# Kernel optimization log

Measured on AMD Instinct MI355X. Metric: run time of the kernel, lower is better.

## Reference

```python
import jax, jax.numpy as jnp
import numpy as np

NUM_CLASSES = 1000
DIM = 256
N = 400000
MOMENTUM = 0.9


def setup_inputs() -> dict:
    key = jax.random.key(0)
    k1, k2, k3 = jax.random.split(key, 3)
    grads = jax.random.normal(k1, (N, DIM), dtype=jnp.float32)
    labels = jax.random.randint(k2, (N,), 0, NUM_CLASSES)
    # centroids buffer in its steady (initialized=True) state
    centroids = jax.random.normal(k3, (NUM_CLASSES, DIM), dtype=jnp.float32) * 0.1
    return {"grads": grads, "labels": labels, "centroids": centroids}


def reference(grads, labels, centroids):
    # --- update_centroids: per-class masked mean + EMA, as one segment-reduce ---
    sums = jax.ops.segment_sum(grads, labels, num_segments=NUM_CLASSES)            # [C, D]
    counts = jax.ops.segment_sum(jnp.ones((grads.shape[0],), grads.dtype), labels,
                                 num_segments=NUM_CLASSES)                          # [C]
    class_means = sums / jnp.maximum(counts, 1.0)[:, None]                          # [C, D]
    present = (counts > 0)[:, None]
    new_centroids = jnp.where(present,
                              MOMENTUM * centroids + (1.0 - MOMENTUM) * class_means,
                              centroids)                                            # classes with no samples keep old centroid

    # --- purify: rank-1 projection removing the first principal direction ---
    centered = new_centroids - new_centroids.mean(axis=0, keepdims=True)            # [C, D]
    _, _, Vh = jnp.linalg.svd(centered, full_matrices=False)
    v_y = Vh[0]                                                                     # [D]
    proj = (grads @ v_y)[:, None] * v_y[None, :]                                    # [N, D]
    return grads - proj
```

## Files before the change

### kernel.cpp

```cpp
#include <hip/hip_runtime.h>

#define N_ROWS 400000
#define DIM 256
#define NCLS 1000
#define NSQ 6
#define NPOLISH 8

#define NB_S 256
#define NT_S 512
#define NBE  64
#define NTE  1024
#define NB_P 2048
#define NT_P 256
#define TOTW_P (NB_P * (NT_P / 64))

typedef float f4 __attribute__((ext_vector_type(4)));

#define OFF_BAR     0
#define OFF_BAR2    64
#define OFF_COUNTS  1024
#define OFF_COLSUM  5120
#define OFF_MAXBUF  6144
#define ZERO_BYTES  6208
#define OFF_BASE    6208
#define OFF_CURSOR  10304
#define OFF_V       14400
#define OFF_IDX     15424
#define OFF_NC      1615424
#define OFF_NCT     2639424
#define OFF_MA      3663424
#define OFF_MB      3925568

template <int NBLK>
__device__ __forceinline__ void grid_bar(unsigned* bar, int& phase) {
  __syncthreads();
  if (threadIdx.x == 0) {
    ++phase;
    __threadfence();
    __hip_atomic_fetch_add(bar, 1u, __ATOMIC_RELAXED, __HIP_MEMORY_SCOPE_AGENT);
    const unsigned target = (unsigned)NBLK * (unsigned)phase;
    while (__hip_atomic_load(bar, __ATOMIC_RELAXED, __HIP_MEMORY_SCOPE_AGENT) < target)
      __builtin_amdgcn_s_sleep(8);
    __threadfence();
  }
  __syncthreads();
}

__global__ __launch_bounds__(NT_S) void k_sort(const int* __restrict__ labels,
                                               char* __restrict__ ws) {
  unsigned* bar    = (unsigned*)(ws + OFF_BAR);
  unsigned* counts = (unsigned*)(ws + OFF_COUNTS);
  unsigned* base   = (unsigned*)(ws + OFF_BASE);
  unsigned* cursor = (unsigned*)(ws + OFF_CURSOR);
  unsigned* idx    = (unsigned*)(ws + OFF_IDX);

  __shared__ unsigned su[1024];
  const int t = threadIdx.x, b = blockIdx.x;
  int phase = 0;

  for (int i = t; i < NCLS; i += NT_S) su[i] = 0u;
  __syncthreads();
  for (int i = b*NT_S + t; i < N_ROWS; i += NB_S*NT_S)
    atomicAdd(&su[labels[i]], 1u);
  __syncthreads();
  for (int i = t; i < NCLS; i += NT_S) { unsigned v = su[i]; if (v) atomicAdd(&counts[i], v); }
  grid_bar<NB_S>(bar, phase);

  if (b == 0) {
    su[t] = counts[t]; su[t+512] = counts[t+512];
    int offset = 1;
    for (int d = 512; d > 0; d >>= 1) {
      __syncthreads();
      if (t < d) { int ai = offset*(2*t+1)-1, bi = offset*(2*t+2)-1; su[bi] += su[ai]; }
      offset <<= 1;
    }
    __syncthreads();
    if (t == 0) su[1023] = 0u;
    for (int d = 1; d < 1024; d <<= 1) {
      offset >>= 1;
      __syncthreads();
      if (t < d) { int ai = offset*(2*t+1)-1, bi = offset*(2*t+2)-1;
                   unsigned tm = su[ai]; su[ai] = su[bi]; su[bi] += tm; }
    }
    __syncthreads();
    base[t] = su[t]; cursor[t] = su[t];
    base[t+512] = su[t+512]; cursor[t+512] = su[t+512];
  }
  grid_bar<NB_S>(bar, phase);

  for (int i = b*NT_S + t; i < N_ROWS; i += NB_S*NT_S) {
    unsigned p = atomicAdd(&cursor[labels[i]], 1u);
    idx[p] = (unsigned)i;
  }
}

__global__ __launch_bounds__(512) void k_reduce(const float* __restrict__ grads,
                                                const unsigned* __restrict__ idx,
                                                const unsigned* __restrict__ base,
                                                const unsigned* __restrict__ counts,
                                                const float* __restrict__ centroids,
                                                float* __restrict__ NC,
                                                float* __restrict__ NCT,
                                                float* __restrict__ colsum) {
  const int cls = blockIdx.x;
  const unsigned s0 = base[cls], n = counts[cls];
  const int wave = threadIdx.x >> 6, lane = threadIdx.x & 63;
  const f4* g4 = (const f4*)grads;
  f4 acc = {0.f, 0.f, 0.f, 0.f};
  unsigned u = (unsigned)wave;
  for (; u + 56 < n; u += 64) {
    unsigned r0 = idx[s0+u],    r1 = idx[s0+u+8];
    unsigned r2 = idx[s0+u+16], r3 = idx[s0+u+24];
    unsigned r4 = idx[s0+u+32], r5 = idx[s0+u+40];
    unsigned r6 = idx[s0+u+48], r7 = idx[s0+u+56];
    f4 a0 = g4[(size_t)r0*64 + lane];
    f4 a1 = g4[(size_t)r1*64 + lane];
    f4 a2 = g4[(size_t)r2*64 + lane];
    f4 a3 = g4[(size_t)r3*64 + lane];
    f4 a4 = g4[(size_t)r4*64 + lane];
    f4 a5 = g4[(size_t)r5*64 + lane];
    f4 a6 = g4[(size_t)r6*64 + lane];
    f4 a7 = g4[(size_t)r7*64 + lane];
    acc += ((a0 + a1) + (a2 + a3)) + ((a4 + a5) + (a6 + a7));
  }
  for (; u < n; u += 8) {
    unsigned r0 = idx[s0+u];
    acc += g4[(size_t)r0*64 + lane];
  }
  __shared__ f4 tmp[8][64];
  tmp[wave][lane] = acc;
  __syncthreads();
  const int d = threadIdx.x;
  if (d < DIM) {
    const float* tf = (const float*)tmp;
    float s = 0.f;
    #pragma unroll
    for (int w2 = 0; w2 < 8; ++w2) s += tf[w2*256 + d];
    float mean = s / fmaxf((float)n, 1.0f);
    float ce = centroids[cls*DIM + d];
    float ncv = (n > 0u) ? (0.9f*ce + 0.1f*mean) : ce;
    NC[cls*DIM + d]  = ncv;
    NCT[d*NCLS + cls] = ncv;
    atomicAdd(&colsum[d], ncv);
  }
}

__global__ __launch_bounds__(NTE) void k_eigen(char* __restrict__ ws) {
  unsigned* bar2   = (unsigned*)(ws + OFF_BAR2);
  float*    colsum = (float*)(ws + OFF_COLSUM);
  unsigned* maxbuf = (unsigned*)(ws + OFF_MAXBUF);
  float*    vfin   = (float*)(ws + OFF_V);
  float*    NC     = (float*)(ws + OFF_NC);
  float*    NCT    = (float*)(ws + OFF_NCT);
  float*    MA     = (float*)(ws + OFF_MA);
  float*    MB     = (float*)(ws + OFF_MB);

  __shared__ float scol[4][NCLS];
  __shared__ float sf[4][NTE];
  __shared__ float sx[DIM], sy[DIM];
  __shared__ int   sidx[256];
  __shared__ unsigned smax;

  const int t = threadIdx.x, b = blockIdx.x;
  const int i = t & 255, h = t >> 8;
  int phase = 0;

  {
    #pragma unroll
    for (int q = 0; q < 4; ++q)
      if (t < NCLS) scol[q][t] = NCT[(size_t)(b + 64*q)*NCLS + t];
    if (t == 0) smax = 0u;
    __syncthreads();
    float a0 = 0.f, a1 = 0.f, a2 = 0.f, a3 = 0.f;
    const int k0 = h * 250;
    #pragma unroll 5
    for (int k = k0; k < k0 + 250; ++k) {
      float nv = NC[k*DIM + i];
      a0 += nv * scol[0][k]; a1 += nv * scol[1][k];
      a2 += nv * scol[2][k]; a3 += nv * scol[3][k];
    }
    sf[0][t] = a0; sf[1][t] = a1; sf[2][t] = a2; sf[3][t] = a3;
    __syncthreads();
    if (h == 0) {
      float am = 0.f;
      #pragma unroll
      for (int q = 0; q < 4; ++q) {
        const int j = b + 64*q;
        float v = sf[q][i]+sf[q][i+256]+sf[q][i+512]+sf[q][i+768]
                - colsum[i]*colsum[j]*(1.0f/NCLS);
        MA[j*DIM + i] = v;
        am = fmaxf(am, fabsf(v));
      }
      #pragma unroll
      for (int m = 1; m < 64; m <<= 1) am = fmaxf(am, __shfl_xor(am, m, 64));
      if ((t & 63) == 0) atomicMax(&smax, __float_as_uint(am));
    }
    __syncthreads();
    if (t == 0) atomicMax(maxbuf, smax);
  }
  grid_bar<NBE>(bar2, phase);

  for (int st = 0; st < NSQ; ++st) {
    const float* A = (st & 1) ? MB : MA;
    float*       C = (st & 1) ? MA : MB;
    const float inv = 1.0f / __uint_as_float(maxbuf[st]);
    #pragma unroll
    for (int q = 0; q < 4; ++q)
      if (t < DIM) scol[q][t] = A[(b + 64*q)*DIM + t];
    if (t == 0) smax = 0u;
    __syncthreads();
    float a0 = 0.f, a1 = 0.f, a2 = 0.f, a3 = 0.f;
    const int k0 = h * 64;
    #pragma unroll 8
    for (int k = k0; k < k0 + 64; ++k) {
      float av = A[k*DIM + i];
      a0 += av * scol[0][k]; a1 += av * scol[1][k];
      a2 += av * scol[2][k]; a3 += av * scol[3][k];
    }
    sf[0][t] = a0; sf[1][t] = a1; sf[2][t] = a2; sf[3][t] = a3;
    __syncthreads();
    if (h == 0) {
      float am = 0.f;
      #pragma unroll
      for (int q = 0; q < 4; ++q) {
        const int j = b + 64*q;
        float v = (sf[q][i]+sf[q][i+256]+sf[q][i+512]+sf[q][i+768]) * inv * inv;
        C[j*DIM + i] = v;
        am = fmaxf(am, fabsf(v));
      }
      #pragma unroll
      for (int m = 1; m < 64; m <<= 1) am = fmaxf(am, __shfl_xor(am, m, 64));
      if ((t & 63) == 0) atomicMax(&smax, __float_as_uint(am));
    }
    __syncthreads();
    if (t == 0) atomicMax(&maxbuf[st+1], smax);
    grid_bar<NBE>(bar2, phase);
  }

  if (b == 0) {
    const int k0 = h * 64;
    float ns = 0.f;
    for (int k = k0; k < k0 + 64; ++k) { float x = MA[k*DIM + i]; ns += x*x; }
    sf[0][t] = ns;
    __syncthreads();
    if (h == 0) {
      scol[0][i] = sf[0][i]+sf[0][i+256]+sf[0][i+512]+sf[0][i+768];
      sidx[i] = i;
    }
    __syncthreads();
    for (int s = 128; s > 0; s >>= 1) {
      if (t < s && scol[0][t+s] > scol[0][t]) { scol[0][t] = scol[0][t+s]; sidx[t] = sidx[t+s]; }
      __syncthreads();
    }
    const int jm = sidx[0];
    const float nrm = sqrtf(fmaxf(scol[0][0], 1e-30f));
    __syncthreads();
    if (t < DIM) sx[t] = MA[(size_t)jm*DIM + t] / nrm;
    __syncthreads();
    for (int it = 0; it < NPOLISH; ++it) {
      float a2 = 0.f;
      #pragma unroll 8
      for (int k = k0; k < k0 + 64; ++k) a2 += MA[k*DIM + i] * sx[k];
      sf[0][t] = a2;
      __syncthreads();
      if (h == 0) {
        float yv = sf[0][i]+sf[0][i+256]+sf[0][i+512]+sf[0][i+768];
        sy[i] = yv;
        float q = yv*yv;
        #pragma unroll
        for (int m = 1; m < 64; m <<= 1) q += __shfl_xor(q, m, 64);
        if ((i & 63) == 0) scol[0][i >> 6] = q;
      }
      __syncthreads();
      const float innrm = rsqrtf(fmaxf(scol[0][0]+scol[0][1]+scol[0][2]+scol[0][3], 1e-30f));
      if (t < DIM) sx[t] = sy[t] * innrm;
      __syncthreads();
    }
    if (t < DIM) vfin[t] = sx[t];
  }
}

__global__ __launch_bounds__(NT_P) void k_project(const f4* __restrict__ g4,
                                                  const float* __restrict__ v,
                                                  f4* __restrict__ out) {
  const int lane = threadIdx.x & 63;
  const f4 v4 = ((const f4*)v)[lane];
  const int w = blockIdx.x * (NT_P/64) + (threadIdx.x >> 6);
  int r = w;
  for (; r + TOTW_P < N_ROWS; r += 2*TOTW_P) {
    f4 a = __builtin_nontemporal_load(&g4[(size_t)r*64 + lane]);
    f4 c = __builtin_nontemporal_load(&g4[(size_t)(r+TOTW_P)*64 + lane]);
    float da = a.x*v4.x + a.y*v4.y + a.z*v4.z + a.w*v4.w;
    float db = c.x*v4.x + c.y*v4.y + c.z*v4.z + c.w*v4.w;
    #pragma unroll
    for (int m = 1; m < 64; m <<= 1) { da += __shfl_xor(da, m, 64); db += __shfl_xor(db, m, 64); }
    f4 o0 = a - da * v4;
    f4 o1 = c - db * v4;
    __builtin_nontemporal_store(o0, &out[(size_t)r*64 + lane]);
    __builtin_nontemporal_store(o1, &out[(size_t)(r+TOTW_P)*64 + lane]);
  }
  for (; r < N_ROWS; r += TOTW_P) {
    f4 a = __builtin_nontemporal_load(&g4[(size_t)r*64 + lane]);
    float da = a.x*v4.x + a.y*v4.y + a.z*v4.z + a.w*v4.w;
    #pragma unroll
    for (int m = 1; m < 64; m <<= 1) da += __shfl_xor(da, m, 64);
    f4 o = a - da * v4;
    __builtin_nontemporal_store(o, &out[(size_t)r*64 + lane]);
  }
}

extern "C" void kernel_launch(void* const* d_in, const int* in_sizes, int n_in,
                              void* d_out, int out_size, void* d_ws, size_t ws_size,
                              hipStream_t stream) {
  const float* grads     = (const float*)d_in[0];
  const int*   labels    = (const int*)d_in[1];
  const float* centroids = (const float*)d_in[2];
  float* out = (float*)d_out;
  char* ws = (char*)d_ws;

  unsigned* idx    = (unsigned*)(ws + OFF_IDX);
  unsigned* counts = (unsigned*)(ws + OFF_COUNTS);
  unsigned* base   = (unsigned*)(ws + OFF_BASE);
  float*    colsum = (float*)(ws + OFF_COLSUM);
  float*    vfin   = (float*)(ws + OFF_V);
  float*    NC     = (float*)(ws + OFF_NC);
  float*    NCT    = (float*)(ws + OFF_NCT);

  (void)hipMemsetAsync(ws, 0, ZERO_BYTES, stream);

  k_sort<<<NB_S, NT_S, 0, stream>>>(labels, ws);
  k_reduce<<<NCLS, 512, 0, stream>>>(grads, idx, base, counts, centroids, NC, NCT, colsum);
  k_eigen<<<NBE, NTE, 0, stream>>>(ws);
  k_project<<<NB_P, NT_P, 0, stream>>>((const f4*)grads, vfin, (f4*)out);
}
```

Before: 440.6 us.

## Spread eigen-solver Gram and squaring over 256 blocks, drop transposed centroid copy

The eigen kernel now runs 256 blocks of 256 threads, each computing one column of the Gram and squared matrices with float4 row loads, instead of 64 blocks of 1024 threads each handling four columns. The transposed centroid buffer written in the reduce kernel is removed, and each block gathers its column with strided reads instead. The aim is to use more compute units for the small matrix products and to cut the scattered transposed writes. In exchange, the grid-wide barriers now wait on four times as many blocks, and the column gathers are uncoalesced.

```diff
diff --git a/kernel.cpp b/kernel.cpp
--- a/kernel.cpp
+++ b/kernel.cpp
@@ -8,8 +8,8 @@
 
 #define NB_S 256
 #define NT_S 512
-#define NBE  64
-#define NTE  1024
+#define NBE  256
+#define NTE  256
 #define NB_P 2048
 #define NT_P 256
 #define TOTW_P (NB_P * (NT_P / 64))
@@ -27,9 +27,8 @@
 #define OFF_V       14400
 #define OFF_IDX     15424
 #define OFF_NC      1615424
-#define OFF_NCT     2639424
-#define OFF_MA      3663424
-#define OFF_MB      3925568
+#define OFF_MA      2639424
+#define OFF_MB      2901568
 
 template <int NBLK>
 __device__ __forceinline__ void grid_bar(unsigned* bar, int& phase) {
@@ -100,7 +99,6 @@
                                                 const unsigned* __restrict__ counts,
                                                 const float* __restrict__ centroids,
                                                 float* __restrict__ NC,
-                                                float* __restrict__ NCT,
                                                 float* __restrict__ colsum) {
   const int cls = blockIdx.x;
   const unsigned s0 = base[cls], n = counts[cls];
@@ -139,8 +137,7 @@
     float mean = s / fmaxf((float)n, 1.0f);
     float ce = centroids[cls*DIM + d];
     float ncv = (n > 0u) ? (0.9f*ce + 0.1f*mean) : ce;
-    NC[cls*DIM + d]  = ncv;
-    NCT[d*NCLS + cls] = ncv;
+    NC[cls*DIM + d] = ncv;
     atomicAdd(&colsum[d], ncv);
   }
 }
@@ -151,132 +148,120 @@
   unsigned* maxbuf = (unsigned*)(ws + OFF_MAXBUF);
   float*    vfin   = (float*)(ws + OFF_V);
   float*    NC     = (float*)(ws + OFF_NC);
-  float*    NCT    = (float*)(ws + OFF_NCT);
   float*    MA     = (float*)(ws + OFF_MA);
   float*    MB     = (float*)(ws + OFF_MB);
 
-  __shared__ float scol[4][NCLS];
-  __shared__ float sf[4][NTE];
-  __shared__ float sx[DIM], sy[DIM];
-  __shared__ int   sidx[256];
-  __shared__ unsigned smax;
+  __shared__ float scol[1024];
+  __shared__ f4    swsum[4][64];
+  __shared__ float sred[256];
+  __shared__ int   sidxs[256];
+  __shared__ float sx[256], sy[256];
 
   const int t = threadIdx.x, b = blockIdx.x;
-  const int i = t & 255, h = t >> 8;
+  const int wave = t >> 6, lane = t & 63;
+  const int j = b;
+  const float* pws = (const float*)swsum;
   int phase = 0;
 
   {
-    #pragma unroll
-    for (int q = 0; q < 4; ++q)
-      if (t < NCLS) scol[q][t] = NCT[(size_t)(b + 64*q)*NCLS + t];
-    if (t == 0) smax = 0u;
-    __syncthreads();
-    float a0 = 0.f, a1 = 0.f, a2 = 0.f, a3 = 0.f;
-    const int k0 = h * 250;
+    for (int k = t; k < NCLS; k += NTE) scol[k] = NC[(size_t)k*DIM + j];
+    __syncthreads();
+    f4 acc = {0,0,0,0};
+    const f4* NC4 = (const f4*)NC;
+    const int k0 = wave * 250;
     #pragma unroll 5
-    for (int k = k0; k < k0 + 250; ++k) {
-      float nv = NC[k*DIM + i];
-      a0 += nv * scol[0][k]; a1 += nv * scol[1][k];
-      a2 += nv * scol[2][k]; a3 += nv * scol[3][k];
-    }
-    sf[0][t] = a0; sf[1][t] = a1; sf[2][t] = a2; sf[3][t] = a3;
-    __syncthreads();
-    if (h == 0) {
-      float am = 0.f;
-      #pragma unroll
-      for (int q = 0; q < 4; ++q) {
-        const int j = b + 64*q;
-        float v = sf[q][i]+sf[q][i+256]+sf[q][i+512]+sf[q][i+768]
-                - colsum[i]*colsum[j]*(1.0f/NCLS);
-        MA[j*DIM + i] = v;
-        am = fmaxf(am, fabsf(v));
-      }
-      #pragma unroll
-      for (int m = 1; m < 64; m <<= 1) am = fmaxf(am, __shfl_xor(am, m, 64));
-      if ((t & 63) == 0) atomicMax(&smax, __float_as_uint(am));
-    }
-    __syncthreads();
-    if (t == 0) atomicMax(maxbuf, smax);
+    for (int k = k0; k < k0 + 250; ++k)
+      acc += NC4[(size_t)k*64 + lane] * scol[k];
+    swsum[wave][lane] = acc;
+    __syncthreads();
+    float v = pws[t] + pws[256+t] + pws[512+t] + pws[768+t]
+            - colsum[t]*colsum[j]*(1.0f/NCLS);
+    MA[(size_t)j*DIM + t] = v;
+    float am = fabsf(v);
+    #pragma unroll
+    for (int m = 1; m < 64; m <<= 1) am = fmaxf(am, __shfl_xor(am, m, 64));
+    __syncthreads();
+    if (lane == 0) sred[wave] = am;
+    __syncthreads();
+    if (t == 0) {
+      float mm = fmaxf(fmaxf(sred[0], sred[1]), fmaxf(sred[2], sred[3]));
+      atomicMax(maxbuf, __float_as_uint(mm));
+    }
   }
   grid_bar<NBE>(bar2, phase);
 
   for (int st = 0; st < NSQ; ++st) {
     const float* A = (st & 1) ? MB : MA;
     float*       C = (st & 1) ? MA : MB;
+    const f4* A4 = (const f4*)A;
     const float inv = 1.0f / __uint_as_float(maxbuf[st]);
-    #pragma unroll
-    for (int q = 0; q < 4; ++q)
-      if (t < DIM) scol[q][t] = A[(b + 64*q)*DIM + t];
-    if (t == 0) smax = 0u;
-    __syncthreads();
-    float a0 = 0.f, a1 = 0.f, a2 = 0.f, a3 = 0.f;
-    const int k0 = h * 64;
+    const float i2 = inv * inv;
+    scol[t] = A[(size_t)t*DIM + j];
+    __syncthreads();
+    f4 acc = {0,0,0,0};
+    const int k0 = wave * 64;
     #pragma unroll 8
-    for (int k = k0; k < k0 + 64; ++k) {
-      float av = A[k*DIM + i];
-      a0 += av * scol[0][k]; a1 += av * scol[1][k];
-      a2 += av * scol[2][k]; a3 += av * scol[3][k];
-    }
-    sf[0][t] = a0; sf[1][t] = a1; sf[2][t] = a2; sf[3][t] = a3;
-    __syncthreads();
-    if (h == 0) {
-      float am = 0.f;
-      #pragma unroll
-      for (int q = 0; q < 4; ++q) {
-        const int j = b + 64*q;
-        float v = (sf[q][i]+sf[q][i+256]+sf[q][i+512]+sf[q][i+768]) * inv * inv;
-        C[j*DIM + i] = v;
-        am = fmaxf(am, fabsf(v));
+    for (int k = k0; k < k0 + 64; ++k)
+      acc += A4[(size_t)k*64 + lane] * scol[k];
+    swsum[wave][lane] = acc;
+    __syncthreads();
+    float v = (pws[t] + pws[256+t] + pws[512+t] + pws[768+t]) * i2;
+    C[(size_t)j*DIM + t] = v;
+    float am = fabsf(v);
+    #pragma unroll
+    for (int m = 1; m < 64; m <<= 1) am = fmaxf(am, __shfl_xor(am, m, 64));
+    __syncthreads();
+    if (lane == 0) sred[wave] = am;
+    __syncthreads();
+    if (t == 0) {
+      float mm = fmaxf(fmaxf(sred[0], sred[1]), fmaxf(sred[2], sred[3]));
+      atomicMax(&maxbuf[st+1], __float_as_uint(mm));
+    }
+    grid_bar<NBE>(bar2, phase);
+  }
+
+  if (b == 0) {
+    const f4* M4 = (const f4*)MA;
+    const int k0 = wave * 64;
+    {
+      f4 na = {0,0,0,0};
+      #pragma unroll 8
+      for (int k = k0; k < k0 + 64; ++k) { f4 av = M4[(size_t)k*64 + lane]; na += av*av; }
+      swsum[wave][lane] = na;
+    }
+    __syncthreads();
+    sred[t] = pws[t] + pws[256+t] + pws[512+t] + pws[768+t];
+    sidxs[t] = t;
+    __syncthreads();
+    for (int s = 128; s > 0; s >>= 1) {
+      if (t < s && sred[t+s] > sred[t]) { sred[t] = sred[t+s]; sidxs[t] = sidxs[t+s]; }
+      __syncthreads();
+    }
+    const int jm = sidxs[0];
+    const float nrm = sqrtf(fmaxf(sred[0], 1e-30f));
+    __syncthreads();
+    sx[t] = MA[(size_t)jm*DIM + t] / nrm;
+    __syncthreads();
+    for (int it = 0; it < NPOLISH; ++it) {
+      f4 ya = {0,0,0,0};
+      #pragma unroll 8
+      for (int k = k0; k < k0 + 64; ++k) ya += M4[(size_t)k*64 + lane] * sx[k];
+      swsum[wave][lane] = ya;
+      __syncthreads();
+      float yv = pws[t] + pws[256+t] + pws[512+t] + pws[768+t];
+      sy[t] = yv;
+      sred[t] = yv*yv;
+      __syncthreads();
+      for (int s = 128; s > 0; s >>= 1) {
+        if (t < s) sred[t] += sred[t+s];
+        __syncthreads();
       }
-      #pragma unroll
-      for (int m = 1; m < 64; m <<= 1) am = fmaxf(am, __shfl_xor(am, m, 64));
-      if ((t & 63) == 0) atomicMax(&smax, __float_as_uint(am));
-    }
-    __syncthreads();
-    if (t == 0) atomicMax(&maxbuf[st+1], smax);
-    grid_bar<NBE>(bar2, phase);
-  }
-
-  if (b == 0) {
-    const int k0 = h * 64;
-    float ns = 0.f;
-    for (int k = k0; k < k0 + 64; ++k) { float x = MA[k*DIM + i]; ns += x*x; }
-    sf[0][t] = ns;
-    __syncthreads();
-    if (h == 0) {
-      scol[0][i] = sf[0][i]+sf[0][i+256]+sf[0][i+512]+sf[0][i+768];
-      sidx[i] = i;
-    }
-    __syncthreads();
-    for (int s = 128; s > 0; s >>= 1) {
-      if (t < s && scol[0][t+s] > scol[0][t]) { scol[0][t] = scol[0][t+s]; sidx[t] = sidx[t+s]; }
-      __syncthreads();
-    }
-    const int jm = sidx[0];
-    const float nrm = sqrtf(fmaxf(scol[0][0], 1e-30f));
-    __syncthreads();
-    if (t < DIM) sx[t] = MA[(size_t)jm*DIM + t] / nrm;
-    __syncthreads();
-    for (int it = 0; it < NPOLISH; ++it) {
-      float a2 = 0.f;
-      #pragma unroll 8
-      for (int k = k0; k < k0 + 64; ++k) a2 += MA[k*DIM + i] * sx[k];
-      sf[0][t] = a2;
-      __syncthreads();
-      if (h == 0) {
-        float yv = sf[0][i]+sf[0][i+256]+sf[0][i+512]+sf[0][i+768];
-        sy[i] = yv;
-        float q = yv*yv;
-        #pragma unroll
-        for (int m = 1; m < 64; m <<= 1) q += __shfl_xor(q, m, 64);
-        if ((i & 63) == 0) scol[0][i >> 6] = q;
-      }
-      __syncthreads();
-      const float innrm = rsqrtf(fmaxf(scol[0][0]+scol[0][1]+scol[0][2]+scol[0][3], 1e-30f));
-      if (t < DIM) sx[t] = sy[t] * innrm;
-      __syncthreads();
-    }
-    if (t < DIM) vfin[t] = sx[t];
+      const float innrm = rsqrtf(fmaxf(sred[0], 1e-30f));
+      __syncthreads();
+      sx[t] = sy[t] * innrm;
+      __syncthreads();
+    }
+    vfin[t] = sx[t];
   }
 }
 
@@ -324,12 +309,11 @@
   float*    colsum = (float*)(ws + OFF_COLSUM);
   float*    vfin   = (float*)(ws + OFF_V);
   float*    NC     = (float*)(ws + OFF_NC);
-  float*    NCT    = (float*)(ws + OFF_NCT);
 
   (void)hipMemsetAsync(ws, 0, ZERO_BYTES, stream);
 
   k_sort<<<NB_S, NT_S, 0, stream>>>(labels, ws);
-  k_reduce<<<NCLS, 512, 0, stream>>>(grads, idx, base, counts, centroids, NC, NCT, colsum);
+  k_reduce<<<NCLS, 512, 0, stream>>>(grads, idx, base, counts, centroids, NC, colsum);
   k_eigen<<<NBE, NTE, 0, stream>>>(ws);
   k_project<<<NB_P, NT_P, 0, stream>>>((const f4*)grads, vfin, (f4*)out);
 }
```

After: 505.0 us. 14.6% more time.
